# Kernel tuning notes

Hardware: AMD Instinct MI355X
Metric: run time of the kernel (lower is better)

## Reference

```python
import jax, jax.numpy as jnp
import numpy as np

K = 5  # filter_size
EPS = 1e-5

def conv1x1(x, w):
    # x: [B,Ci,H,W], w: [Co,Ci]
    return jnp.einsum('bihw,oi->bohw', x, w)

def layernorm_c(x, g, b):
    # LayerNorm over channel dim of NCHW (torch permutes to NHWC, norms last dim)
    m = x.mean(axis=1, keepdims=True)
    v = x.var(axis=1, keepdims=True)
    xn = (x - m) / jnp.sqrt(v + EPS)
    return xn * g[None, :, None, None] + b[None, :, None, None]

def conv3x3(x, w):
    return jax.lax.conv_general_dilated(x, w, (1, 1), [(1, 1), (1, 1)],
                                        dimension_numbers=('NCHW', 'OIHW', 'NCHW'))

def apply_dyn_filter(feat, filt):
    # feat: [B,C,H,W]; filt: [B,C*K*K,H,W] ordered as C x (K*K row-major), matching
    # torch .view(B,C,K*K,H,W) and F.unfold channel layout.
    B, C, H, W = feat.shape
    f = filt.reshape(B, C, K * K, H, W)
    p = K // 2
    fp = jnp.pad(feat, ((0, 0), (0, 0), (p, p), (p, p)))  # zero pad, same as F.unfold
    out = jnp.zeros_like(feat)
    for ki in range(K):
        for kj in range(K):
            out = out + fp[:, :, ki:ki + H, kj:kj + W] * f[:, :, ki * K + kj]
    return out


def setup_inputs() -> dict:
    key = jax.random.key(0)
    ks = jax.random.split(key, 9)
    B, Cin, H, W = 1, 64, 128, 128
    Ch = 128
    s = lambda fan: 1.0 / np.sqrt(fan)
    inp = {
        'rgb_high': jax.random.normal(ks[0], (B, Cin, H, W), jnp.float32),
        'event':    jax.random.normal(ks[1], (B, Cin, H, W), jnp.float32),
        'conv_w':   jax.random.normal(ks[2], (Ch, Cin), jnp.float32) * s(Cin),
        'ln_g':     jnp.ones((Ch,), jnp.float32),
        'ln_b':     jnp.zeros((Ch,), jnp.float32),
        'df1_w':    jax.random.normal(ks[3], (Ch, Ch, 3, 3), jnp.float32) * s(Ch * 9),
        'df2_w':    jax.random.normal(ks[4], (Ch * K * K, Ch), jnp.float32) * s(Ch),
        'sp_w':     jax.random.normal(ks[5], (Ch, Ch), jnp.float32) * s(Ch),
        'out_w':    jax.random.normal(ks[6], (Cin, Ch), jnp.float32) * s(Ch),
    }
    return inp


def reference(rgb_high, event, conv_w, ln_g, ln_b, df1_w, df2_w, sp_w, out_w):
    rgb_feat = layernorm_c(conv1x1(rgb_high, conv_w), ln_g, ln_b)
    ev_feat = layernorm_c(conv1x1(event, conv_w), ln_g, ln_b)
    # dynamic filter generator: conv3x3 -> ReLU -> conv1x1 (shared weights)
    rgb_filter = conv1x1(jax.nn.relu(conv3x3(rgb_feat, df1_w)), df2_w)
    ev_filter = conv1x1(jax.nn.relu(conv3x3(ev_feat, df1_w)), df2_w)
    rgb_en = apply_dyn_filter(rgb_feat, rgb_filter)
    ev_en = apply_dyn_filter(ev_feat, ev_filter)
    rgb_filtered = rgb_en * jax.nn.sigmoid(conv1x1(ev_en, sp_w))
    rgb_fused = rgb_en + rgb_filtered + rgb_feat
    rgb_norm = layernorm_c(rgb_fused, ln_g, ln_b)
    return conv1x1(rgb_norm, out_w)
```

## Files before the change

### kernel.cpp

```cpp
#include <hip/hip_runtime.h>
#include <math.h>

#define HW 16384
#define WD 128
#define HD 128
#define CIN 64
#define CH 128
#define EPSV 1e-5f

typedef __attribute__((ext_vector_type(8))) short short8;
typedef __attribute__((ext_vector_type(4))) short short4v;
typedef __attribute__((ext_vector_type(4))) float f32x4;

__device__ __forceinline__ short f2bf(float x) {
  unsigned u = __float_as_uint(x);
  u += 0x7FFFu + ((u >> 16) & 1u);
  return (short)(u >> 16);
}
__device__ __forceinline__ float bf2f(short x) {
  return __uint_as_float(((unsigned)(unsigned short)x) << 16);
}

__global__ __launch_bounds__(256) void k_prep_misc(
    const float* __restrict__ cw, const float* __restrict__ w3,
    const float* __restrict__ spw, const float* __restrict__ outw,
    const float* __restrict__ rgb, const float* __restrict__ ev,
    short* __restrict__ cwp, short* __restrict__ w3p,
    short* __restrict__ spwp, short* __restrict__ outwp,
    short* __restrict__ xT_rgb, short* __restrict__ xT_ev) {
  int idx = blockIdx.x * 256 + threadIdx.x;
  if (idx < 8192) {
    int j = idx & 7, grp = (idx >> 3) & 3, m = (idx >> 5) & 127, q = idx >> 12;
    cwp[idx] = f2bf(cw[m * CIN + q * 32 + grp * 8 + j]);
  } else if (idx < 155648) {
    int i = idx - 8192;
    int j = i & 7, grp = (i >> 3) & 3, m = (i >> 5) & 127, ks = i >> 12;
    int tap = ks >> 2, q = ks & 3;
    int c = q * 32 + grp * 8 + j;
    w3p[i] = f2bf(w3[(m * CH + c) * 9 + tap]);
  } else if (idx < 172032) {
    int i = idx - 155648;
    int j = i & 7, grp = (i >> 3) & 3, m = (i >> 5) & 127, q = i >> 12;
    spwp[i] = f2bf(spw[m * CH + q * 32 + grp * 8 + j]);
  } else if (idx < 180224) {
    int i = idx - 172032;
    int j = i & 7, grp = (i >> 3) & 3, m = (i >> 5) & 63, q = i >> 11;
    outwp[i] = f2bf(outw[m * CH + q * 32 + grp * 8 + j]);
  } else {
    int i = idx - 180224;
    int img = i >> 14, p = i & 16383;
    const float* x = img ? ev : rgb;
    short* xT = img ? xT_ev : xT_rgb;
#pragma unroll
    for (int cb = 0; cb < 8; ++cb) {
      short8 v;
#pragma unroll
      for (int j = 0; j < 8; ++j) v[j] = f2bf(x[(cb * 8 + j) * HW + p]);
      *(short8*)(xT + p * CIN + cb * 8) = v;
    }
  }
}

__global__ __launch_bounds__(256) void k_prep_df2(const float* __restrict__ df2,
                                                  short* __restrict__ df2p) {
  int idx = blockIdx.x * 256 + threadIdx.x;
  int j = idx & 7;
  int slotp = (idx >> 3) & 511;
  int c = idx >> 12;
  int t = slotp >> 4, k8l = slotp & 15;
  int k8 = k8l ^ (t & 7);
  float v = (t < 25) ? df2[(c * 25 + t) * CH + k8 * 8 + j] : 0.f;
  df2p[idx] = f2bf(v);
}

__global__ __launch_bounds__(256) void k_feat_mfma(
    const short* __restrict__ xT_rgb, const short* __restrict__ xT_ev,
    const short* __restrict__ cwp, const float* __restrict__ g,
    const float* __restrict__ b,
    short* __restrict__ featT_rgb, short* __restrict__ featT_ev) {
  __shared__ float sg[CH], sb[CH];
  int tid = threadIdx.x;
  if (tid < CH) { sg[tid] = g[tid]; sb[tid] = b[tid]; }
  __syncthreads();
  const short* xT = blockIdx.z ? xT_ev : xT_rgb;
  short* featT = blockIdx.z ? featT_ev : featT_rgb;
  int wave = tid >> 6, lane = tid & 63, col = lane & 15, grp = lane >> 4;
  int p = blockIdx.x * 64 + wave * 16 + col;

  const short8* bp = (const short8*)(xT + p * CIN);
  short8 bq0 = bp[grp], bq1 = bp[4 + grp];
  const short8* ap = (const short8*)cwp;

  f32x4 acc[8];
#pragma unroll
  for (int mt = 0; mt < 8; ++mt) {
    acc[mt] = (f32x4){0.f, 0.f, 0.f, 0.f};
    short8 a0 = ap[(0 * 128 + mt * 16 + col) * 4 + grp];
    short8 a1 = ap[(1 * 128 + mt * 16 + col) * 4 + grp];
    acc[mt] = __builtin_amdgcn_mfma_f32_16x16x32_bf16(a0, bq0, acc[mt], 0, 0, 0);
    acc[mt] = __builtin_amdgcn_mfma_f32_16x16x32_bf16(a1, bq1, acc[mt], 0, 0, 0);
  }
  float s = 0.f, s2 = 0.f;
#pragma unroll
  for (int mt = 0; mt < 8; ++mt)
#pragma unroll
    for (int r = 0; r < 4; ++r) { float v = acc[mt][r]; s += v; s2 += v * v; }
  s += __shfl_xor(s, 16);  s += __shfl_xor(s, 32);
  s2 += __shfl_xor(s2, 16); s2 += __shfl_xor(s2, 32);
  float mean = s * (1.f / CH);
  float var = s2 * (1.f / CH) - mean * mean;
  float rinv = rsqrtf(var + EPSV);
#pragma unroll
  for (int mt = 0; mt < 8; ++mt) {
    short4v fv;
#pragma unroll
    for (int r = 0; r < 4; ++r) {
      int m = mt * 16 + grp * 4 + r;
      fv[r] = f2bf((acc[mt][r] - mean) * rinv * sg[m] + sb[m]);
    }
    *(short4v*)(featT + p * CH + mt * 16 + grp * 4) = fv;
  }
}

__global__ __launch_bounds__(256) void k_conv3_v3(
    const short* __restrict__ featT_rgb, const short* __restrict__ featT_ev,
    const short* __restrict__ w3p,
    short* __restrict__ rT_rgb, short* __restrict__ rT_ev) {
  const short* featT = blockIdx.z ? featT_ev : featT_rgb;
  short* rT = blockIdx.z ? rT_ev : rT_rgb;
  int tid = threadIdx.x, wave = tid >> 6, lane = tid & 63;
  int col = lane & 15, grp = lane >> 4;
  int mh = wave & 1;
  int ty = (blockIdx.x >> 3) * 4 + (wave >> 1) * 2;
  int tx = (blockIdx.x & 7) * 16;
  int x = tx + col;

  f32x4 acc[2][4];
#pragma unroll
  for (int s = 0; s < 2; ++s)
#pragma unroll
    for (int mt = 0; mt < 4; ++mt) acc[s][mt] = (f32x4){0.f, 0.f, 0.f, 0.f};

  const short8* ap = (const short8*)w3p;
#pragma unroll
  for (int ks = 0; ks < 36; ++ks) {
    const int tap = ks >> 2, q = ks & 3;
    const int dy = tap / 3 - 1, dx = tap % 3 - 1;
    int xs = x + dx;
    bool xok = (unsigned)xs < (unsigned)WD;
    int y0 = ty + dy, y1 = ty + 1 + dy;
    short8 b0 = {0, 0, 0, 0, 0, 0, 0, 0}, b1 = {0, 0, 0, 0, 0, 0, 0, 0};
    if (xok && (unsigned)y0 < (unsigned)HD)
      b0 = *(const short8*)(featT + (y0 * WD + xs) * CH + q * 32 + grp * 8);
    if (xok && (unsigned)y1 < (unsigned)HD)
      b1 = *(const short8*)(featT + (y1 * WD + xs) * CH + q * 32 + grp * 8);
#pragma unroll
    for (int mt = 0; mt < 4; ++mt) {
      short8 a = ap[(ks * 128 + (mh * 4 + mt) * 16 + col) * 4 + grp];
      acc[0][mt] = __builtin_amdgcn_mfma_f32_16x16x32_bf16(a, b0, acc[0][mt], 0, 0, 0);
      acc[1][mt] = __builtin_amdgcn_mfma_f32_16x16x32_bf16(a, b1, acc[1][mt], 0, 0, 0);
    }
  }
#pragma unroll
  for (int s = 0; s < 2; ++s) {
    int p = (ty + s) * WD + x;
#pragma unroll
    for (int mt = 0; mt < 4; ++mt) {
      short4v v;
#pragma unroll
      for (int r = 0; r < 4; ++r) v[r] = f2bf(fmaxf(acc[s][mt][r], 0.f));
      *(short4v*)(rT + p * CH + (mh * 4 + mt) * 16 + grp * 4) = v;
    }
  }
}

__global__ __launch_bounds__(256, 3) void k_filt_v6(
    const short* __restrict__ featT_rgb, const short* __restrict__ featT_ev,
    const short* __restrict__ rT_rgb, const short* __restrict__ rT_ev,
    const short* __restrict__ df2p,
    short* __restrict__ enT_rgb, short* __restrict__ enT_ev) {
  __shared__ short lsA[4 * 512 * 8];
  __shared__ float fwv[4 * 400 + 64];
  const short* featT = blockIdx.z ? featT_ev : featT_rgb;
  const short* rT = blockIdx.z ? rT_ev : rT_rgb;
  short* enT = blockIdx.z ? enT_ev : enT_rgb;
  int tid = threadIdx.x;
  int wave = tid >> 6, lane = tid & 63;
  int col = lane & 15, grp = lane >> 4;
  int ty0 = (blockIdx.x >> 3) * 16, tx0 = (blockIdx.x & 7) * 16;
  int c0 = blockIdx.y * 4;
  int py0 = ty0 + wave * 4;
  int pxx = tx0 + col;

  {
    const short8* gsrc = (const short8*)(df2p + (size_t)c0 * 4096);
    short8* lA = (short8*)lsA;
    for (int i = tid; i < 2048; i += 256) lA[i] = gsrc[i];
  }
  for (int px = tid; px < 400; px += 256) {
    int wr = px / 20, wc = px % 20;
    int y = ty0 + wr - 2, x = tx0 + wc - 2;
    short4v v = {0, 0, 0, 0};
    if ((unsigned)y < (unsigned)HD && (unsigned)x < (unsigned)WD)
      v = *(const short4v*)(featT + (y * WD + x) * CH + c0);
#pragma unroll
    for (int ci = 0; ci < 4; ++ci) fwv[ci * 400 + px] = bf2f(v[ci]);
  }
  if (tid < 64) fwv[4 * 400 + tid] = 0.f;

  short8 rv[4][4];
#pragma unroll
  for (int s = 0; s < 4; ++s) {
    const short8* bp = (const short8*)(rT + ((py0 + s) * WD + pxx) * CH);
#pragma unroll
    for (int q = 0; q < 4; ++q) rv[s][q] = bp[q * 4 + grp];
  }
#pragma unroll
  for (int s = 0; s < 4; ++s)
#pragma unroll
    for (int q = 0; q < 4; ++q) asm volatile("" :: "v"(rv[s][q]));

  int idx0[4], idx1[4];
#pragma unroll
  for (int r = 0; r < 4; ++r) {
    int tap0 = grp * 4 + r;
    int tap1 = 16 + grp * 4 + r;
    idx0[r] = (wave * 4 + tap0 / 5) * 20 + col + tap0 % 5;
    idx1[r] = (wave * 4 + tap1 / 5) * 20 + col + tap1 % 5;
  }
  __syncthreads();

  const short8* lA8 = (const short8*)lsA;
  short* stp = enT + ((py0 + grp) * WD + pxx) * CH + c0;
  short4v sv;

#pragma unroll
  for (int c = 0; c < 4; ++c) {
    int base0 = c * 512 + col * 16;
    int base1 = base0 + 256;
    short8 a[4];
    f32x4 acc0[4], acc1[4];
#pragma unroll
    for (int q = 0; q < 4; ++q) a[q] = lA8[base0 + (((q << 2) | grp) ^ (col & 7))];
#pragma unroll
    for (int s = 0; s < 4; ++s) {
      acc0[s] = (f32x4){0.f, 0.f, 0.f, 0.f};
#pragma unroll
      for (int q = 0; q < 4; ++q)
        acc0[s] = __builtin_amdgcn_mfma_f32_16x16x32_bf16(a[q], rv[s][q], acc0[s], 0, 0, 0);
    }
#pragma unroll
    for (int q = 0; q < 4; ++q) a[q] = lA8[base1 + (((q << 2) | grp) ^ (col & 7))];
#pragma unroll
    for (int s = 0; s < 4; ++s) {
      acc1[s] = (f32x4){0.f, 0.f, 0.f, 0.f};
#pragma unroll
      for (int q = 0; q < 4; ++q)
        acc1[s] = __builtin_amdgcn_mfma_f32_16x16x32_bf16(a[q], rv[s][q], acc1[s], 0, 0, 0);
    }
    const float* fwc = fwv + c * 400;
    float part[4];
#pragma unroll
    for (int s = 0; s < 4; ++s) {
      float p = 0.f;
#pragma unroll
      for (int r = 0; r < 4; ++r) {
        p += fwc[idx0[r] + s * 20] * acc0[s][r];
        p += fwc[idx1[r] + s * 20] * acc1[s][r];
      }
      part[s] = p;
    }
#pragma unroll
    for (int s = 0; s < 4; ++s) part[s] += __shfl_xor(part[s], 16);
#pragma unroll
    for (int s = 0; s < 4; ++s) part[s] += __shfl_xor(part[s], 32);
    float val = (grp == 0) ? part[0] : (grp == 1) ? part[1]
              : (grp == 2) ? part[2] : part[3];
    sv[c] = f2bf(val);
  }
  *(short4v*)stp = sv;
}

__global__ __launch_bounds__(256) void k_post(
    const short* __restrict__ enT_rgb, const short* __restrict__ enT_ev,
    const short* __restrict__ featT_rgb,
    const short* __restrict__ spwp, const short* __restrict__ outwp,
    const float* __restrict__ g, const float* __restrict__ b,
    float* __restrict__ out) {
  __shared__ short nlds[4][16 * 136];
  __shared__ float sg[CH], sb[CH];
  int tid = threadIdx.x;
  if (tid < CH) { sg[tid] = g[tid]; sb[tid] = b[tid]; }
  __syncthreads();
  int wave = tid >> 6, lane = tid & 63, col = lane & 15, grp = lane >> 4;
  int p = blockIdx.x * 64 + wave * 16 + col;

  const short8* bp = (const short8*)(enT_ev + p * CH);
  short8 bq[4];
#pragma unroll
  for (int q = 0; q < 4; ++q) bq[q] = bp[q * 4 + grp];
  const short8* ap = (const short8*)spwp;
  f32x4 z[8];
#pragma unroll
  for (int mt = 0; mt < 8; ++mt) {
    z[mt] = (f32x4){0.f, 0.f, 0.f, 0.f};
#pragma unroll
    for (int q = 0; q < 4; ++q)
      z[mt] = __builtin_amdgcn_mfma_f32_16x16x32_bf16(
          ap[(q * 128 + mt * 16 + col) * 4 + grp], bq[q], z[mt], 0, 0, 0);
  }

  const short4v* er = (const short4v*)(enT_rgb + p * CH);
  const short4v* fr = (const short4v*)(featT_rgb + p * CH);
  float fused[8][4];
  float s = 0.f, s2 = 0.f;
#pragma unroll
  for (int mt = 0; mt < 8; ++mt) {
    short4v e4 = er[mt * 4 + grp];
    short4v f4 = fr[mt * 4 + grp];
#pragma unroll
    for (int r = 0; r < 4; ++r) {
      float sig = 1.f / (1.f + __expf(-z[mt][r]));
      float f = bf2f(e4[r]) * (1.f + sig) + bf2f(f4[r]);
      fused[mt][r] = f; s += f; s2 += f * f;
    }
  }
  s += __shfl_xor(s, 16);  s += __shfl_xor(s, 32);
  s2 += __shfl_xor(s2, 16); s2 += __shfl_xor(s2, 32);
  float mean = s * (1.f / CH);
  float var = s2 * (1.f / CH) - mean * mean;
  float rinv = rsqrtf(var + EPSV);

  short* nl = &nlds[wave][0];
#pragma unroll
  for (int mt = 0; mt < 8; ++mt) {
    short4v nv;
#pragma unroll
    for (int r = 0; r < 4; ++r) {
      int o = mt * 16 + grp * 4 + r;
      nv[r] = f2bf((fused[mt][r] - mean) * rinv * sg[o] + sb[o]);
    }
    *(short4v*)(nl + col * 136 + mt * 16 + grp * 4) = nv;
  }

  short8 nb[4];
#pragma unroll
  for (int q = 0; q < 4; ++q)
    nb[q] = *(const short8*)(nl + col * 136 + q * 32 + grp * 8);
  const short8* op = (const short8*)outwp;
#pragma unroll
  for (int mt = 0; mt < 4; ++mt) {
    f32x4 oacc = {0.f, 0.f, 0.f, 0.f};
#pragma unroll
    for (int q = 0; q < 4; ++q)
      oacc = __builtin_amdgcn_mfma_f32_16x16x32_bf16(
          op[(q * 64 + mt * 16 + col) * 4 + grp], nb[q], oacc, 0, 0, 0);
#pragma unroll
    for (int r = 0; r < 4; ++r)
      out[(mt * 16 + grp * 4 + r) * HW + p] = oacc[r];
  }
}

extern "C" void kernel_launch(void* const* d_in, const int* in_sizes, int n_in,
                              void* d_out, int out_size, void* d_ws, size_t ws_size,
                              hipStream_t stream) {
  const float* rgb  = (const float*)d_in[0];
  const float* ev   = (const float*)d_in[1];
  const float* cw   = (const float*)d_in[2];
  const float* g    = (const float*)d_in[3];
  const float* b    = (const float*)d_in[4];
  const float* w3   = (const float*)d_in[5];
  const float* df2  = (const float*)d_in[6];
  const float* spw  = (const float*)d_in[7];
  const float* outw = (const float*)d_in[8];
  float* out = (float*)d_out;
  char* wsb = (char*)d_ws;

  const size_t MB = 1u << 20;
  short* featT_rgb = (short*)(wsb);
  short* featT_ev  = (short*)(wsb + 4 * MB);
  short* rT_rgb    = (short*)(wsb + 8 * MB);
  short* rT_ev     = (short*)(wsb + 12 * MB);
  short* enT_rgb   = (short*)(wsb + 16 * MB);
  short* enT_ev    = (short*)(wsb + 20 * MB);
  short* xT_rgb    = (short*)(wsb + 24 * MB);
  short* xT_ev     = (short*)(wsb + 26 * MB);
  short* df2p      = (short*)(wsb + 28 * MB);
  short* w3p       = (short*)(wsb + 29 * MB);
  short* cwp       = (short*)(wsb + 30 * MB);
  short* spwp      = (short*)(wsb + 31 * MB);
  short* outwp     = (short*)(wsb + 32 * MB);

  hipLaunchKernelGGL(k_prep_misc, dim3(832), dim3(256), 0, stream,
                     cw, w3, spw, outw, rgb, ev,
                     cwp, w3p, spwp, outwp, xT_rgb, xT_ev);
  hipLaunchKernelGGL(k_prep_df2, dim3(2048), dim3(256), 0, stream, df2, df2p);
  hipLaunchKernelGGL(k_feat_mfma, dim3(256, 1, 2), dim3(256), 0, stream,
                     xT_rgb, xT_ev, cwp, g, b, featT_rgb, featT_ev);
  hipLaunchKernelGGL(k_conv3_v3, dim3(256, 1, 2), dim3(256), 0, stream,
                     featT_rgb, featT_ev, w3p, rT_rgb, rT_ev);
  hipLaunchKernelGGL(k_filt_v6, dim3(64, 32, 2), dim3(256), 0, stream,
                     featT_rgb, featT_ev, rT_rgb, rT_ev, df2p, enT_rgb, enT_ev);
  hipLaunchKernelGGL(k_post, dim3(256), dim3(256), 0, stream,
                     enT_rgb, enT_ev, featT_rgb, spwp, outwp, g, b, out);
}
```

Baseline: 115.1 us.

## Stage conv3x3 halo tile in LDS and regroup filter taps for contiguous reads

The 3x3 conv kernel now loads an 18x6 halo tile of features into XOR-swizzled shared memory once per block and reads the MFMA B operands from LDS, instead of issuing bounds-checked global loads for every tap. The dynamic-filter kernel reorders the df2 weight rows so each MFMA output group holds four consecutive taps along a row or column. It also stores a transposed copy of the feature window in LDS, so the per-tap weighting can use contiguous base+offset reads in place of per-register index arrays. This adds LDS usage and a sync in conv3, and doubles the feature window LDS in the filter kernel, which may affect occupancy.

New measurement: 135.3 us. +17.6%, slower.

```diff
diff --git a/kernel.cpp b/kernel.cpp
--- a/kernel.cpp
+++ b/kernel.cpp
@@ -67,9 +67,20 @@
   int j = idx & 7;
   int slotp = (idx >> 3) & 511;
   int c = idx >> 12;
-  int t = slotp >> 4, k8l = slotp & 15;
-  int k8 = k8l ^ (t & 7);
-  float v = (t < 25) ? df2[(c * 25 + t) * CH + k8 * 8 + j] : 0.f;
+  int ms = slotp >> 4, k8l = slotp & 15;
+  int k8 = k8l ^ (ms & 7);
+  int k = k8 * 8 + j;
+  int t;
+  if (ms < 16) {
+    t = (ms >> 2) * 5 + (ms & 3);
+  } else {
+    int g = (ms >> 2) & 3, r = ms & 3;
+    if (g == 0) t = 20 + r;
+    else if (g == 1) t = r * 5 + 4;
+    else if (g == 2 && r == 0) t = 24;
+    else t = -1;
+  }
+  float v = (t >= 0) ? df2[(c * 25 + t) * CH + k] : 0.f;
   df2p[idx] = f2bf(v);
 }
 
@@ -122,19 +133,32 @@
   }
 }
 
-__global__ __launch_bounds__(256) void k_conv3_v3(
+__global__ __launch_bounds__(256) void k_conv3_v4(
     const short* __restrict__ featT_rgb, const short* __restrict__ featT_ev,
     const short* __restrict__ w3p,
     short* __restrict__ rT_rgb, short* __restrict__ rT_ev) {
+  __shared__ short sF[108 * 128];
   const short* featT = blockIdx.z ? featT_ev : featT_rgb;
   short* rT = blockIdx.z ? rT_ev : rT_rgb;
   int tid = threadIdx.x, wave = tid >> 6, lane = tid & 63;
   int col = lane & 15, grp = lane >> 4;
+  int ty0 = (blockIdx.x >> 3) * 4;
+  int tx0 = (blockIdx.x & 7) * 16;
+
+  short8* sF8w = (short8*)sF;
+  for (int i = tid; i < 1728; i += 256) {
+    int ksl = i & 15, px = i >> 4;
+    int yl = px / 18, xl = px % 18;
+    int y = ty0 - 1 + yl, x = tx0 - 1 + xl;
+    short8 v = {0, 0, 0, 0, 0, 0, 0, 0};
+    if ((unsigned)y < (unsigned)HD && (unsigned)x < (unsigned)WD)
+      v = *(const short8*)(featT + (y * WD + x) * CH + ksl * 8);
+    sF8w[px * 16 + (ksl ^ (xl & 7))] = v;
+  }
+  __syncthreads();
+
   int mh = wave & 1;
-  int ty = (blockIdx.x >> 3) * 4 + (wave >> 1) * 2;
-  int tx = (blockIdx.x & 7) * 16;
-  int x = tx + col;
-
+  int wty = (wave >> 1) * 2;
   f32x4 acc[2][4];
 #pragma unroll
   for (int s = 0; s < 2; ++s)
@@ -142,18 +166,16 @@
     for (int mt = 0; mt < 4; ++mt) acc[s][mt] = (f32x4){0.f, 0.f, 0.f, 0.f};
 
   const short8* ap = (const short8*)w3p;
+  const short8* sF8 = (const short8*)sF;
 #pragma unroll
   for (int ks = 0; ks < 36; ++ks) {
     const int tap = ks >> 2, q = ks & 3;
     const int dy = tap / 3 - 1, dx = tap % 3 - 1;
-    int xs = x + dx;
-    bool xok = (unsigned)xs < (unsigned)WD;
-    int y0 = ty + dy, y1 = ty + 1 + dy;
-    short8 b0 = {0, 0, 0, 0, 0, 0, 0, 0}, b1 = {0, 0, 0, 0, 0, 0, 0, 0};
-    if (xok && (unsigned)y0 < (unsigned)HD)
-      b0 = *(const short8*)(featT + (y0 * WD + xs) * CH + q * 32 + grp * 8);
-    if (xok && (unsigned)y1 < (unsigned)HD)
-      b1 = *(const short8*)(featT + (y1 * WD + xs) * CH + q * 32 + grp * 8);
+    int xl = col + dx + 1;
+    int sl = (q * 4 + grp) ^ (xl & 7);
+    int yl0 = wty + dy + 1;
+    short8 b0 = sF8[(yl0 * 18 + xl) * 16 + sl];
+    short8 b1 = sF8[((yl0 + 1) * 18 + xl) * 16 + sl];
 #pragma unroll
     for (int mt = 0; mt < 4; ++mt) {
       short8 a = ap[(ks * 128 + (mh * 4 + mt) * 16 + col) * 4 + grp];
@@ -163,7 +185,7 @@
   }
 #pragma unroll
   for (int s = 0; s < 2; ++s) {
-    int p = (ty + s) * WD + x;
+    int p = (ty0 + wty + s) * WD + tx0 + col;
 #pragma unroll
     for (int mt = 0; mt < 4; ++mt) {
       short4v v;
@@ -174,13 +196,13 @@
   }
 }
 
-__global__ __launch_bounds__(256, 3) void k_filt_v6(
+__global__ __launch_bounds__(256, 3) void k_filt_v8(
     const short* __restrict__ featT_rgb, const short* __restrict__ featT_ev,
     const short* __restrict__ rT_rgb, const short* __restrict__ rT_ev,
     const short* __restrict__ df2p,
     short* __restrict__ enT_rgb, short* __restrict__ enT_ev) {
   __shared__ short lsA[4 * 512 * 8];
-  __shared__ float fwv[4 * 400 + 64];
+  __shared__ float fwall[2 * 4 * 408];
   const short* featT = blockIdx.z ? featT_ev : featT_rgb;
   const short* rT = blockIdx.z ? rT_ev : rT_rgb;
   short* enT = blockIdx.z ? enT_ev : enT_rgb;
@@ -204,9 +226,16 @@
     if ((unsigned)y < (unsigned)HD && (unsigned)x < (unsigned)WD)
       v = *(const short4v*)(featT + (y * WD + x) * CH + c0);
 #pragma unroll
-    for (int ci = 0; ci < 4; ++ci) fwv[ci * 400 + px] = bf2f(v[ci]);
-  }
-  if (tid < 64) fwv[4 * 400 + tid] = 0.f;
+    for (int ci = 0; ci < 4; ++ci) {
+      float f = bf2f(v[ci]);
+      fwall[ci * 408 + wr * 20 + wc] = f;
+      fwall[1632 + ci * 408 + wc * 20 + wr] = f;
+    }
+  }
+  if (tid < 64) {
+    int copy = tid >> 5, cc = (tid >> 3) & 3, k = tid & 7;
+    fwall[copy * 1632 + cc * 408 + 400 + k] = 0.f;
+  }
 
   short8 rv[4][4];
 #pragma unroll
@@ -220,14 +249,14 @@
 #pragma unroll
     for (int q = 0; q < 4; ++q) asm volatile("" :: "v"(rv[s][q]));
 
-  int idx0[4], idx1[4];
-#pragma unroll
-  for (int r = 0; r < 4; ++r) {
-    int tap0 = grp * 4 + r;
-    int tap1 = 16 + grp * 4 + r;
-    idx0[r] = (wave * 4 + tap0 / 5) * 20 + col + tap0 % 5;
-    idx1[r] = (wave * 4 + tap1 / 5) * 20 + col + tap1 % 5;
-  }
+  int rowb = wave * 4;
+  int base0 = (rowb + grp) * 20 + col;
+  int step1 = (grp == 1) ? 1 : 20;
+  int base1;
+  if (grp == 0)      base1 = (rowb + 4) * 20 + col;
+  else if (grp == 1) base1 = 1632 + (col + 4) * 20 + rowb;
+  else if (grp == 2) base1 = (rowb + 4) * 20 + col + 4;
+  else               base1 = rowb * 20 + col;
   __syncthreads();
 
   const short8* lA8 = (const short8*)lsA;
@@ -236,12 +265,12 @@
 
 #pragma unroll
   for (int c = 0; c < 4; ++c) {
-    int base0 = c * 512 + col * 16;
-    int base1 = base0 + 256;
+    int base0c = c * 512 + col * 16;
+    int base1c = base0c + 256;
     short8 a[4];
     f32x4 acc0[4], acc1[4];
 #pragma unroll
-    for (int q = 0; q < 4; ++q) a[q] = lA8[base0 + (((q << 2) | grp) ^ (col & 7))];
+    for (int q = 0; q < 4; ++q) a[q] = lA8[base0c + (((q << 2) | grp) ^ (col & 7))];
 #pragma unroll
     for (int s = 0; s < 4; ++s) {
       acc0[s] = (f32x4){0.f, 0.f, 0.f, 0.f};
@@ -250,7 +279,7 @@
         acc0[s] = __builtin_amdgcn_mfma_f32_16x16x32_bf16(a[q], rv[s][q], acc0[s], 0, 0, 0);
     }
 #pragma unroll
-    for (int q = 0; q < 4; ++q) a[q] = lA8[base1 + (((q << 2) | grp) ^ (col & 7))];
+    for (int q = 0; q < 4; ++q) a[q] = lA8[base1c + (((q << 2) | grp) ^ (col & 7))];
 #pragma unroll
     for (int s = 0; s < 4; ++s) {
       acc1[s] = (f32x4){0.f, 0.f, 0.f, 0.f};
@@ -258,16 +287,16 @@
       for (int q = 0; q < 4; ++q)
         acc1[s] = __builtin_amdgcn_mfma_f32_16x16x32_bf16(a[q], rv[s][q], acc1[s], 0, 0, 0);
     }
-    const float* fwc = fwv + c * 400;
+    int cb = c * 408;
     float part[4];
 #pragma unroll
     for (int s = 0; s < 4; ++s) {
-      float p = 0.f;
-#pragma unroll
-      for (int r = 0; r < 4; ++r) {
-        p += fwc[idx0[r] + s * 20] * acc0[s][r];
-        p += fwc[idx1[r] + s * 20] * acc1[s][r];
-      }
+      int i0 = cb + base0 + s * 20;
+      int i1 = cb + base1 + s * step1;
+      float p = fwall[i0] * acc0[s][0] + fwall[i0 + 1] * acc0[s][1]
+              + fwall[i0 + 2] * acc0[s][2] + fwall[i0 + 3] * acc0[s][3]
+              + fwall[i1] * acc1[s][0] + fwall[i1 + 1] * acc1[s][1]
+              + fwall[i1 + 2] * acc1[s][2] + fwall[i1 + 3] * acc1[s][3];
       part[s] = p;
     }
 #pragma unroll
@@ -397,9 +426,9 @@
   hipLaunchKernelGGL(k_prep_df2, dim3(2048), dim3(256), 0, stream, df2, df2p);
   hipLaunchKernelGGL(k_feat_mfma, dim3(256, 1, 2), dim3(256), 0, stream,
                      xT_rgb, xT_ev, cwp, g, b, featT_rgb, featT_ev);
-  hipLaunchKernelGGL(k_conv3_v3, dim3(256, 1, 2), dim3(256), 0, stream,
+  hipLaunchKernelGGL(k_conv3_v4, dim3(256, 1, 2), dim3(256), 0, stream,
                      featT_rgb, featT_ev, w3p, rT_rgb, rT_ev);
-  hipLaunchKernelGGL(k_filt_v6, dim3(64, 32, 2), dim3(256), 0, stream,
+  hipLaunchKernelGGL(k_filt_v8, dim3(64, 32, 2), dim3(256), 0, stream,
                      featT_rgb, featT_ev, rT_rgb, rT_ev, df2p, enT_rgb, enT_ev);
   hipLaunchKernelGGL(k_post, dim3(256), dim3(256), 0, stream,
                      enT_rgb, enT_ev, featT_rgb, spwp, outwp, g, b, out);
```
